# Kernel optimization log

Measured on AMD Instinct MI355X. Metric: run time of the kernel, lower is better.

Reference implementation:

```python
import jax, jax.numpy as jnp
import numpy as np
from jax import lax

B, IN_N, MID_N, OUT_N, K, L, WH = 16, 256, 256, 256, 3, 4096, 1024
EPS = 1e-5


def att_conv(x, W, b=None):
    # x: [B, Cin, L], W: [B, Cout, Cin, K] -> per-sample conv1d, padding='same'
    pl, pr = (K - 1) // 2, K // 2
    xp = jnp.pad(x, ((0, 0), (0, 0), (pl, pr)))
    out = 0.
    for t in range(K):  # small fixed K, unrolled shifted-slice einsum
        out = out + jnp.einsum('bcl,boc->bol', lax.dynamic_slice_in_dim(xp, t, L, 2), W[..., t])
    if b is not None:
        out = out + b[:, :, None]
    return out


def batch_norm(x, w, b):
    # training-mode BN over (N, L) per channel, biased variance
    mean = x.mean((0, 2), keepdims=True)
    var = ((x - mean) ** 2).mean((0, 2), keepdims=True)
    return (x - mean) * (w[None, :, None] / jnp.sqrt(var + EPS)) + b[None, :, None]


def se_module(x, w1, b1, w2, b2):
    s = x.mean(2, keepdims=True)  # [B, C, 1]
    s = jax.nn.relu(jnp.einsum('bcl,oc->bol', s, w1) + b1[None, :, None])
    s = jax.nn.sigmoid(jnp.einsum('bcl,oc->bol', s, w2) + b2[None, :, None])
    return x * s


def setup_inputs() -> dict:
    key = jax.random.key(0)
    ks = jax.random.split(key, 16)
    f = lambda k, sh, sc=0.02: jax.random.normal(k, sh, jnp.float32) * sc
    return {
        'x': f(ks[0], (B, IN_N, L), 1.0),
        'att1': f(ks[1], (B, MID_N, WH), 1.0),
        'att2': f(ks[2], (B, MID_N, WH), 1.0),
        'att3': f(ks[3], (B, OUT_N, WH), 1.0),
        'w1_w': f(ks[4], (IN_N * K, WH)), 'w1_b': jnp.zeros((IN_N * K,), jnp.float32),
        'w2_w': f(ks[5], (MID_N * K, WH)), 'w2_b': jnp.zeros((MID_N * K,), jnp.float32),
        'w3_w': f(ks[6], (MID_N * K, WH)), 'w3_b': jnp.zeros((MID_N * K,), jnp.float32),
        'b1_w': f(ks[7], (1, WH)), 'b1_b': jnp.zeros((1,), jnp.float32),
        'bn2_w': jnp.full((MID_N,), 0.1, jnp.float32), 'bn2_b': jnp.zeros((MID_N,), jnp.float32),
        'bn3_w': jnp.full((OUT_N,), 0.1, jnp.float32), 'bn3_b': jnp.zeros((OUT_N,), jnp.float32),
        'se1_w': f(ks[8], (OUT_N, OUT_N)), 'se1_b': jnp.zeros((OUT_N,), jnp.float32),
        'se2_w': f(ks[9], (OUT_N, OUT_N)), 'se2_b': jnp.zeros((OUT_N,), jnp.float32),
    }


def reference(x, att1, att2, att3, w1_w, w1_b, w2_w, w2_b, w3_w, w3_b,
              b1_w, b1_b, bn2_w, bn2_b, bn3_w, bn3_b, se1_w, se1_b, se2_w, se2_b):
    shortcut = x  # in_n == out_n, no downsample -> Identity
    # hypernetwork weight generation (Linear on last dim)
    W1 = (att1 @ w1_w.T + w1_b).reshape(B, MID_N, IN_N, K)
    W2 = (att2 @ w2_w.T + w2_b).reshape(B, MID_N, MID_N, K)
    W3 = (att3 @ w3_w.T + w3_b).reshape(B, OUT_N, MID_N, K)
    b1 = (att1 @ b1_w.T + b1_b)[..., 0]  # [B, mid_n]
    h = jax.nn.relu(att_conv(x, W1, b1))
    h = jax.nn.relu(batch_norm(att_conv(h, W2), bn2_w, bn2_b))
    h = jax.nn.relu(batch_norm(att_conv(h, W3), bn3_w, bn3_b))
    out = jax.nn.relu(se_module(h, se1_w, se1_b, se2_w, se2_b) + shortcut)
    return out
```

## Files before the change

### kernel.cpp

```cpp
#include <hip/hip_runtime.h>
#include <hip/hip_bf16.h>

using bf16 = __hip_bfloat16;
typedef __attribute__((ext_vector_type(4))) float f32x4;
typedef __attribute__((ext_vector_type(8))) short short8;
typedef __attribute__((ext_vector_type(2))) unsigned int uint2v;
typedef __attribute__((ext_vector_type(4))) unsigned int uint4v;

#define DEVI static __device__ __forceinline__

DEVI unsigned short f2b(float f){
  unsigned int u = __float_as_uint(f);
  unsigned int r = (u + 0x7fffu + ((u >> 16) & 1u)) >> 16;
  return (unsigned short)r;
}
DEVI float b2f(unsigned short u){
  return __uint_as_float(((unsigned int)u) << 16);
}

DEVI void gload16(const void* g, void* l){
  __builtin_amdgcn_global_load_lds(
      (const __attribute__((address_space(1))) unsigned int*)g,
      (__attribute__((address_space(3))) unsigned int*)l, 16, 0, 0);
}

__global__ __launch_bounds__(256) void k_transpose_x(const float* __restrict__ x,
                                                     bf16* __restrict__ xt)
{
  __shared__ float tile[64][65];
  const int b = blockIdx.z, l0 = blockIdx.x*64, c0 = blockIdx.y*64;
  const int tid = threadIdx.x;
  {
    const int r = tid >> 2, q = tid & 3;
    const float* src = x + ((size_t)(b*256 + c0 + r))*4096 + l0 + q*16;
    #pragma unroll
    for (int j = 0; j < 4; ++j){
      const f32x4 v = *reinterpret_cast<const f32x4*>(src + j*4);
      #pragma unroll
      for (int e = 0; e < 4; ++e) tile[r][q*16 + j*4 + e] = v[e];
    }
  }
  __syncthreads();
  {
    const int jr = tid >> 2, cq = tid & 3;
    unsigned int w[8];
    #pragma unroll
    for (int e = 0; e < 8; ++e){
      const float lo = tile[cq*16 + 2*e][jr];
      const float hi = tile[cq*16 + 2*e + 1][jr];
      w[e] = (unsigned int)f2b(lo) | ((unsigned int)f2b(hi) << 16);
    }
    unsigned short* dst = (unsigned short*)xt + ((size_t)b*4098 + l0 + jr + 1)*256 + c0 + cq*16;
    uint4v a0 = {w[0],w[1],w[2],w[3]}, a1 = {w[4],w[5],w[6],w[7]};
    *reinterpret_cast<uint4v*>(dst)     = a0;
    *reinterpret_cast<uint4v*>(dst + 8) = a1;
  }
}

__global__ void k_zero_pads(bf16* __restrict__ xt, bf16* __restrict__ h1t)
{
  const int b = blockIdx.x, tid = threadIdx.x;
  const size_t top = (size_t)b*4098*256 + tid;
  const size_t bot = (size_t)b*4098*256 + (size_t)4097*256 + tid;
  unsigned short* px = (unsigned short*)xt;
  unsigned short* ph = (unsigned short*)h1t;
  px[top] = 0; px[bot] = 0; ph[top] = 0; ph[bot] = 0;
}

__global__ __launch_bounds__(256) void k_cvt3(const float* __restrict__ s0, const float* __restrict__ s1,
                                              const float* __restrict__ s2, bf16* __restrict__ dst, int n1)
{
  const size_t total = (size_t)3 * (size_t)n1 / 4;
  for (size_t i = (size_t)blockIdx.x*256 + threadIdx.x; i < total; i += (size_t)gridDim.x*256){
    const size_t e = i*4;
    const int which = (int)(e / (size_t)n1);
    const size_t off = e - (size_t)which*(size_t)n1;
    const float* s = which==0 ? s0 : which==1 ? s1 : s2;
    const f32x4 v = *reinterpret_cast<const f32x4*>(s + off);
    uint2v p;
    p[0] = (unsigned)f2b(v[0]) | ((unsigned)f2b(v[1])<<16);
    p[1] = (unsigned)f2b(v[2]) | ((unsigned)f2b(v[3])<<16);
    *reinterpret_cast<uint2v*>((unsigned short*)dst + e) = p;
  }
}

__global__ __launch_bounds__(256, 3) void k_gen(const float* __restrict__ att1f, const float* __restrict__ att2f,
                                                const float* __restrict__ att3f, const bf16* __restrict__ wbp,
                                                const float* __restrict__ bias0, const float* __restrict__ bias1,
                                                const float* __restrict__ bias2, bf16* __restrict__ Wt)
{
  __shared__ bf16 sAll[24576];
  const int flat = blockIdx.x + blockIdx.z*64;
  const int xcd = flat & 7, s = flat >> 3;
  const int t = s % 3, u = s / 3;
  const int ch = u & 1;
  const int tau = (u >> 1)*8 + xcd;
  const int i = tau >> 5, boc = tau & 31;
  const int bo0 = boc*128, c0 = ch*128;
  const bf16*  __restrict__ A  = wbp + (size_t)i*768*1024 + (size_t)(c0*3 + t)*1024;
  const float* __restrict__ Bf = ((i==0) ? att1f : (i==1) ? att2f : att3f) + (size_t)bo0*1024;
  const float* __restrict__ bias = (i==0) ? bias0 : (i==1) ? bias1 : bias2;
  const int tid = threadIdx.x, lane = tid & 63, wid = tid >> 6;
  const int wr = wid >> 1, wc = wid & 1;
  const int frow = lane & 15, g = lane >> 4;
  f32x4 acc[4][4] = {};

#define GEN_STAGE(kt, bufi) { \
    _Pragma("unroll") \
    for (int j = 0; j < 2; ++j){ \
      const int q = tid + j*256, r = q >> 2, s3 = q & 3; \
      const int cc = (s3 ^ ((r >> 1) & 3)) * 8; \
      gload16(A + (size_t)r*3072 + (kt)*32 + cc, (char*)sAll + (bufi)*8192 + q*16); \
    } \
    _Pragma("unroll") \
    for (int j = 0; j < 4; ++j){ \
      const int q = tid + j*256, r = q >> 3, s7 = q & 7; \
      const int ss = s7 ^ (r & 7); \
      gload16(Bf + (size_t)r*1024 + (kt)*32 + ss*4, (char*)sAll + 16384 + (bufi)*16384 + q*16); \
    } \
  }

  GEN_STAGE(0, 0);
  #pragma unroll 1
  for (int kt = 0; kt < 32; ++kt){
    const int p = kt & 1;
    if (kt + 1 < 32){
      GEN_STAGE(kt+1, p^1);
      asm volatile("s_waitcnt vmcnt(6)" ::: "memory");
    } else {
      asm volatile("s_waitcnt vmcnt(0)" ::: "memory");
    }
    __builtin_amdgcn_s_barrier();
    const char* pA = (const char*)sAll + p*8192;
    const char* pB = (const char*)sAll + 16384 + p*16384;
    short8 bfr[4];
    #pragma unroll
    for (int n = 0; n < 4; ++n){
      const int row = wc*64 + n*16 + frow;
      const f32x4 f0 = *reinterpret_cast<const f32x4*>(pB + row*128 + (((2*g)  ^ (row & 7))*16));
      const f32x4 f1 = *reinterpret_cast<const f32x4*>(pB + row*128 + (((2*g+1)^ (row & 7))*16));
      unsigned int w0, w1, w2, w3;
      asm("v_cvt_pk_bf16_f32 %0, %1, %2" : "=v"(w0) : "v"(f0[0]), "v"(f0[1]));
      asm("v_cvt_pk_bf16_f32 %0, %1, %2" : "=v"(w1) : "v"(f0[2]), "v"(f0[3]));
      asm("v_cvt_pk_bf16_f32 %0, %1, %2" : "=v"(w2) : "v"(f1[0]), "v"(f1[1]));
      asm("v_cvt_pk_bf16_f32 %0, %1, %2" : "=v"(w3) : "v"(f1[2]), "v"(f1[3]));
      union { uint4v u; short8 sv; } cvtu;
      cvtu.u[0] = w0; cvtu.u[1] = w1; cvtu.u[2] = w2; cvtu.u[3] = w3;
      bfr[n] = cvtu.sv;
    }
    __builtin_amdgcn_s_setprio(1);
    #pragma unroll
    for (int m = 0; m < 4; ++m){
      const int row = wr*64 + m*16 + frow;
      const int sl = g ^ ((row >> 1) & 3);
      const short8 af = *reinterpret_cast<const short8*>(pA + row*64 + sl*16);
      #pragma unroll
      for (int n = 0; n < 4; ++n)
        acc[m][n] = __builtin_amdgcn_mfma_f32_16x16x32_bf16(af, bfr[n], acc[m][n], 0, 0, 0);
    }
    __builtin_amdgcn_s_setprio(0);
    __builtin_amdgcn_s_barrier();
  }
#undef GEN_STAGE

  #pragma unroll
  for (int m = 0; m < 4; ++m){
    const int lcol = wr*64 + m*16 + g*4;
    float bi[4];
    #pragma unroll
    for (int j = 0; j < 4; ++j) bi[j] = bias[(c0 + lcol + j)*3 + t];
    #pragma unroll
    for (int n = 0; n < 4; ++n){
      const int row = wc*64 + n*16 + frow;
      uint2v pk;
      pk[0] = (unsigned)f2b(acc[m][n][0] + bi[0]) | ((unsigned)f2b(acc[m][n][1] + bi[1]) << 16);
      pk[1] = (unsigned)f2b(acc[m][n][2] + bi[2]) | ((unsigned)f2b(acc[m][n][3] + bi[3]) << 16);
      const int chunk = (lcol >> 3) ^ (row & 15);
      *reinterpret_cast<uint2v*>((char*)sAll + row*256 + chunk*16 + (g&1)*8) = pk;
    }
  }
  __syncthreads();
  {
    const int bb = boc >> 1, o0 = (boc & 1)*128;
    char* gp = (char*)Wt + 2*(((((size_t)(i*16 + bb)*3 + t)*256 + o0)*256) + c0);
    #pragma unroll
    for (int it = 0; it < 8; ++it){
      const int row = it*16 + (tid >> 4);
      const int c = tid & 15;
      const int cs2 = c ^ (row & 15);
      const uint4v v = *reinterpret_cast<const uint4v*>((const char*)sAll + row*256 + cs2*16);
      *reinterpret_cast<uint4v*>(gp + (size_t)row*512 + c*16) = v;
    }
  }
}

__global__ __launch_bounds__(256) void k_b1(const float* __restrict__ att1, const float* __restrict__ b1w,
                                            const float* __restrict__ b1b, float* __restrict__ out)
{
  const int m = blockIdx.x*4 + (threadIdx.x >> 6);
  const int lane = threadIdx.x & 63;
  const float* a = att1 + (size_t)m*1024;
  float s = 0.f;
  for (int k = lane*4; k < 1024; k += 256){
    const f32x4 v = *reinterpret_cast<const f32x4*>(a + k);
    const f32x4 w = *reinterpret_cast<const f32x4*>(b1w + k);
    s += v[0]*w[0] + v[1]*w[1] + v[2]*w[2] + v[3]*w[3];
  }
  #pragma unroll
  for (int d = 32; d > 0; d >>= 1) s += __shfl_down(s, d);
  if (lane == 0) out[m] = s + b1b[0];
}

__global__ __launch_bounds__(512, 4) void k_conv(const bf16* __restrict__ Xt, const bf16* __restrict__ W,
                                                 const float* __restrict__ bias, bf16* __restrict__ out,
                                                 int outBatchStride, int outRowOff, int applyRelu,
                                                 float* __restrict__ statSum, float* __restrict__ statSq)
{
  __shared__ bf16 sAll[32768];
  const int flat = blockIdx.x + (blockIdx.z << 5);
  const int xcd = flat & 7, slot = flat >> 3;
  const int b = 2*xcd + (slot >> 5);
  const int l0 = (slot & 31) * 128;
  const int tid = threadIdx.x, lane = tid & 63, wid = tid >> 6;
  const int wr = wid >> 1, wc = wid & 1;
  const int frow = lane & 15, g = lane >> 4;
  f32x4 acc[4][4] = {};

#define CONV_STAGE(kt, bufi) { \
    const int ct3 = (kt)/3, tt = (kt) - ct3*3, c0 = ct3*32; \
    const bf16* Ab = W  + (((size_t)b*3 + tt)*256)*256 + c0; \
    const bf16* Bb = Xt + ((size_t)b*4098 + l0 + tt)*256 + c0; \
    _Pragma("unroll") \
    for (int j = 0; j < 2; ++j){ \
      const int q = tid + j*512, r = q >> 2, s3 = q & 3; \
      const int cc = (s3 ^ ((r >> 1) & 3)) * 8; \
      gload16(Ab + (size_t)r*256 + cc, &sAll[(bufi)*8192 + q*8]); \
    } \
    { const int q = tid, r = q >> 2, s3 = q & 3; \
      const int cc = (s3 ^ ((r >> 1) & 3)) * 8; \
      gload16(Bb + (size_t)r*256 + cc, &sAll[16384 + (bufi)*4096 + q*8]); } \
  }

  CONV_STAGE(0, 0);
  #pragma unroll 1
  for (int kt = 0; kt < 24; ++kt){
    const int buf = kt & 1;
    if (kt + 1 < 24){
      CONV_STAGE(kt+1, buf^1);
      asm volatile("s_waitcnt vmcnt(3)" ::: "memory");
    } else {
      asm volatile("s_waitcnt vmcnt(0)" ::: "memory");
    }
    __builtin_amdgcn_s_barrier();
    const bf16* pA = sAll + buf*8192;
    const bf16* pB = sAll + 16384 + buf*4096;
    short8 bfr[4], afr[4];
    #pragma unroll
    for (int n = 0; n < 4; ++n){
      const int row = wc*64 + n*16 + frow;
      const int sl = g ^ ((row >> 1) & 3);
      bfr[n] = *reinterpret_cast<const short8*>(pB + row*32 + sl*8);
    }
    #pragma unroll
    for (int m = 0; m < 4; ++m){
      const int row = wr*64 + m*16 + frow;
      const int sl = g ^ ((row >> 1) & 3);
      afr[m] = *reinterpret_cast<const short8*>(pA + row*32 + sl*8);
    }
    __builtin_amdgcn_s_setprio(1);
    #pragma unroll
    for (int m = 0; m < 4; ++m)
      #pragma unroll
      for (int n = 0; n < 4; ++n)
        acc[m][n] = __builtin_amdgcn_mfma_f32_16x16x32_bf16(afr[m], bfr[n], acc[m][n], 0, 0, 0);
    __builtin_amdgcn_s_setprio(0);
    __builtin_amdgcn_s_barrier();
  }
#undef CONV_STAGE

  float cs[4][4] = {{0.f}}, cq[4][4] = {{0.f}};
  #pragma unroll
  for (int m = 0; m < 4; ++m){
    const int col = wr*64 + m*16 + g*4;
    float bi[4] = {0.f, 0.f, 0.f, 0.f};
    if (bias){
      const f32x4 bv = *reinterpret_cast<const f32x4*>(bias + b*256 + col);
      bi[0]=bv[0]; bi[1]=bv[1]; bi[2]=bv[2]; bi[3]=bv[3];
    }
    #pragma unroll
    for (int n = 0; n < 4; ++n){
      const int row = wc*64 + n*16 + frow;
      float v[4];
      #pragma unroll
      for (int j = 0; j < 4; ++j){
        v[j] = acc[m][n][j] + bi[j];
        if (applyRelu) v[j] = fmaxf(v[j], 0.f);
        cs[m][j] += v[j];
        cq[m][j] += v[j]*v[j];
      }
      uint2v pk;
      pk[0] = (unsigned)f2b(v[0]) | ((unsigned)f2b(v[1]) << 16);
      pk[1] = (unsigned)f2b(v[2]) | ((unsigned)f2b(v[3]) << 16);
      const int chunk = (col >> 3) ^ (row & 31);
      *reinterpret_cast<uint2v*>((char*)sAll + row*512 + chunk*16 + (g&1)*8) = pk;
    }
  }
  __syncthreads();
  {
    char* gp = (char*)out + 2*((size_t)b*outBatchStride + (size_t)(l0 + outRowOff)*256);
    #pragma unroll
    for (int it = 0; it < 8; ++it){
      const int row = it*16 + (tid >> 5);
      const int c = tid & 31;
      const int cs2 = c ^ (row & 31);
      const uint4v v = *reinterpret_cast<const uint4v*>((const char*)sAll + row*512 + cs2*16);
      *reinterpret_cast<uint4v*>(gp + (size_t)row*512 + c*16) = v;
    }
  }
  if (statSum){
    #pragma unroll
    for (int m = 0; m < 4; ++m)
      #pragma unroll
      for (int j = 0; j < 4; ++j){
        #pragma unroll
        for (int d = 1; d < 16; d <<= 1){
          cs[m][j] += __shfl_xor(cs[m][j], d);
          cq[m][j] += __shfl_xor(cq[m][j], d);
        }
      }
    __syncthreads();
    float* ls = (float*)sAll;
    float* lq = ls + 512;
    if (frow == 0){
      #pragma unroll
      for (int m = 0; m < 4; ++m)
        #pragma unroll
        for (int j = 0; j < 4; ++j){
          ls[wid*64 + m*16 + g*4 + j] = cs[m][j];
          lq[wid*64 + m*16 + g*4 + j] = cq[m][j];
        }
    }
    __syncthreads();
    if (tid < 256){
      const int o = tid, wrI = o >> 6, idx = o & 63;
      const float s  = ls[(wrI*2 + 0)*64 + idx] + ls[(wrI*2 + 1)*64 + idx];
      const float qq = lq[(wrI*2 + 0)*64 + idx] + lq[(wrI*2 + 1)*64 + idx];
      atomicAdd(statSum + o, s);
      atomicAdd(statSq  + o, qq);
    }
  }
}

__global__ void k_bnfin(const float* __restrict__ sum, const float* __restrict__ sq,
                        const float* __restrict__ g, const float* __restrict__ bb,
                        float* __restrict__ scale, float* __restrict__ shift)
{
  const int o = threadIdx.x;
  const float inv = 1.f/65536.f;
  const float m = sum[o]*inv;
  const float v = fmaxf(sq[o]*inv - m*m, 0.f);
  const float sc = g[o] / sqrtf(v + 1e-5f);
  scale[o] = sc;
  shift[o] = bb[o] - m*sc;
}

__global__ __launch_bounds__(256) void k_norm2(const bf16* __restrict__ y, const float* __restrict__ scale,
                                               const float* __restrict__ shift, bf16* __restrict__ h)
{
  const int gr = blockIdx.x*8 + (threadIdx.x >> 5);
  const int oc = threadIdx.x & 31;
  const int b = gr / 4098, lp = gr - b*4098;
  unsigned short* dst = (unsigned short*)h + (size_t)gr*256 + oc*8;
  if (lp == 0 || lp == 4097){
    uint4v z = {0u,0u,0u,0u};
    *reinterpret_cast<uint4v*>(dst) = z;
    return;
  }
  const unsigned short* src = (const unsigned short*)y + ((size_t)b*4096 + (lp-1))*256 + oc*8;
  const uint4v in = *reinterpret_cast<const uint4v*>(src);
  const f32x4 sA0 = *reinterpret_cast<const f32x4*>(scale + oc*8);
  const f32x4 sA1 = *reinterpret_cast<const f32x4*>(scale + oc*8 + 4);
  const f32x4 hA0 = *reinterpret_cast<const f32x4*>(shift + oc*8);
  const f32x4 hA1 = *reinterpret_cast<const f32x4*>(shift + oc*8 + 4);
  uint4v ov;
  #pragma unroll
  for (int e = 0; e < 4; ++e){
    const unsigned int w = in[e];
    const float sc0 = (e<2) ? sA0[2*e] : sA1[2*e-4];
    const float sc1 = (e<2) ? sA0[2*e+1] : sA1[2*e-3];
    const float sh0 = (e<2) ? hA0[2*e] : hA1[2*e-4];
    const float sh1 = (e<2) ? hA0[2*e+1] : hA1[2*e-3];
    const float v0 = fmaxf(b2f((unsigned short)(w & 0xffffu))*sc0 + sh0, 0.f);
    const float v1 = fmaxf(b2f((unsigned short)(w >> 16))*sc1 + sh1, 0.f);
    ov[e] = (unsigned)f2b(v0) | ((unsigned)f2b(v1) << 16);
  }
  *reinterpret_cast<uint4v*>(dst) = ov;
}

__global__ __launch_bounds__(256) void k_norm3(bf16* __restrict__ y, const float* __restrict__ scale,
                                               const float* __restrict__ shift, float* __restrict__ s_sum)
{
  __shared__ float red[8][256];
  const int tid = threadIdx.x;
  const int rr = tid >> 5, oc = tid & 31;
  const size_t row = (size_t)blockIdx.x*8 + rr;
  const int b = (int)(row >> 12);
  unsigned short* p = (unsigned short*)y + row*256 + oc*8;
  const uint4v in = *reinterpret_cast<const uint4v*>(p);
  const f32x4 sA0 = *reinterpret_cast<const f32x4*>(scale + oc*8);
  const f32x4 sA1 = *reinterpret_cast<const f32x4*>(scale + oc*8 + 4);
  const f32x4 hA0 = *reinterpret_cast<const f32x4*>(shift + oc*8);
  const f32x4 hA1 = *reinterpret_cast<const f32x4*>(shift + oc*8 + 4);
  uint4v ov;
  float loc[8];
  #pragma unroll
  for (int e = 0; e < 4; ++e){
    const unsigned int w = in[e];
    const float sc0 = (e<2) ? sA0[2*e] : sA1[2*e-4];
    const float sc1 = (e<2) ? sA0[2*e+1] : sA1[2*e-3];
    const float sh0 = (e<2) ? hA0[2*e] : hA1[2*e-4];
    const float sh1 = (e<2) ? hA0[2*e+1] : hA1[2*e-3];
    const float v0 = fmaxf(b2f((unsigned short)(w & 0xffffu))*sc0 + sh0, 0.f);
    const float v1 = fmaxf(b2f((unsigned short)(w >> 16))*sc1 + sh1, 0.f);
    loc[2*e] = v0; loc[2*e+1] = v1;
    ov[e] = (unsigned)f2b(v0) | ((unsigned)f2b(v1) << 16);
  }
  *reinterpret_cast<uint4v*>(p) = ov;
  #pragma unroll
  for (int j = 0; j < 8; ++j) red[rr][oc*8 + j] = loc[j];
  __syncthreads();
  const int o = tid;
  float tot = 0.f;
  #pragma unroll
  for (int r2 = 0; r2 < 8; ++r2) tot += red[r2][o];
  atomicAdd(&s_sum[(size_t)b*256 + o], tot);
}

__global__ __launch_bounds__(256) void k_se(const float* __restrict__ s_sum, const float* __restrict__ w1,
                                            const float* __restrict__ b1, const float* __restrict__ w2,
                                            const float* __restrict__ b2, float* __restrict__ s2)
{
  __shared__ float sv[256];
  __shared__ float t1[256];
  const int b = blockIdx.x, o = threadIdx.x;
  sv[o] = s_sum[(size_t)b*256 + o] * (1.f/4096.f);
  __syncthreads();
  float a = b1[o];
  for (int c = 0; c < 256; ++c) a += w1[(size_t)o*256 + c] * sv[c];
  t1[o] = fmaxf(a, 0.f);
  __syncthreads();
  float a2 = b2[o];
  for (int c = 0; c < 256; ++c) a2 += w2[(size_t)o*256 + c] * t1[c];
  s2[(size_t)b*256 + o] = 1.f / (1.f + expf(-a2));
}

__global__ __launch_bounds__(256) void k_final(const bf16* __restrict__ h3, const float* __restrict__ s2,
                                               const float* __restrict__ x, float* __restrict__ out)
{
  __shared__ float tile[64][65];
  const int b = blockIdx.z, o0 = blockIdx.y*64, l0 = blockIdx.x*64;
  const int tid = threadIdx.x;
  {
    const int r = tid >> 2, q = tid & 3;
    const unsigned short* src = (const unsigned short*)h3 + ((size_t)b*4096 + l0 + r)*256 + o0 + q*16;
    const uint4v a0 = *reinterpret_cast<const uint4v*>(src);
    const uint4v a1 = *reinterpret_cast<const uint4v*>(src + 8);
    #pragma unroll
    for (int e = 0; e < 4; ++e){
      tile[r][q*16 + 2*e]         = b2f((unsigned short)(a0[e] & 0xffffu));
      tile[r][q*16 + 2*e + 1]     = b2f((unsigned short)(a0[e] >> 16));
      tile[r][q*16 + 8 + 2*e]     = b2f((unsigned short)(a1[e] & 0xffffu));
      tile[r][q*16 + 8 + 2*e + 1] = b2f((unsigned short)(a1[e] >> 16));
    }
  }
  __syncthreads();
  {
    const int orow = tid >> 2, q = tid & 3;
    const int o = o0 + orow;
    const float sc = s2[(size_t)b*256 + o];
    const float* xs = x + ((size_t)b*256 + o)*4096 + l0 + q*16;
    float* dst = out + ((size_t)b*256 + o)*4096 + l0 + q*16;
    #pragma unroll
    for (int k = 0; k < 16; k += 4){
      const f32x4 xv = *reinterpret_cast<const f32x4*>(xs + k);
      f32x4 r;
      #pragma unroll
      for (int e = 0; e < 4; ++e)
        r[e] = fmaxf(tile[q*16 + k + e][orow]*sc + xv[e], 0.f);
      *reinterpret_cast<f32x4*>(dst + k) = r;
    }
  }
}

extern "C" void kernel_launch(void* const* d_in, const int* in_sizes, int n_in,
                              void* d_out, int out_size, void* d_ws, size_t ws_size,
                              hipStream_t stream)
{
  const float* x     = (const float*)d_in[0];
  const float* att1  = (const float*)d_in[1];
  const float* att2  = (const float*)d_in[2];
  const float* att3  = (const float*)d_in[3];
  const float* w1_w  = (const float*)d_in[4];
  const float* w1_b  = (const float*)d_in[5];
  const float* w2_w  = (const float*)d_in[6];
  const float* w2_b  = (const float*)d_in[7];
  const float* w3_w  = (const float*)d_in[8];
  const float* w3_b  = (const float*)d_in[9];
  const float* b1_w  = (const float*)d_in[10];
  const float* b1_b  = (const float*)d_in[11];
  const float* bn2_w = (const float*)d_in[12];
  const float* bn2_b = (const float*)d_in[13];
  const float* bn3_w = (const float*)d_in[14];
  const float* bn3_b = (const float*)d_in[15];
  const float* se1_w = (const float*)d_in[16];
  const float* se1_b = (const float*)d_in[17];
  const float* se2_w = (const float*)d_in[18];
  const float* se2_b = (const float*)d_in[19];

  char* ws = (char*)d_ws;
  bf16*  xT   = (bf16*)(ws + 0);
  bf16*  h1T  = (bf16*)(ws + 33570816);
  bf16*  y2T  = (bf16*)(ws + 67141632);
  bf16*  h2T  = (bf16*)(ws + 100696064);
  bf16*  Wt   = (bf16*)(ws + 134266880);
  bf16*  wb   = (bf16*)(ws + 178307072);
  float* b1v  = (float*)(ws + 183025664);
  float* st   = (float*)(ws + 183042048);
  float* bn2sum = st;
  float* bn2sq  = st + 256;
  float* bn3sum = st + 512;
  float* bn3sq  = st + 768;
  float* s_sum  = st + 1024;
  float* scale2 = st + 5120;
  float* shift2 = st + 5376;
  float* scale3 = st + 5632;
  float* shift3 = st + 5888;
  float* s2v    = st + 6144;
  bf16*  y3T  = (bf16*)(ws + 0);

  hipMemsetAsync(st, 0, 5120*sizeof(float), stream);

  k_transpose_x<<<dim3(64,4,16),256,0,stream>>>(x, xT);
  k_zero_pads<<<16,256,0,stream>>>(xT, h1T);
  k_cvt3<<<512,256,0,stream>>>(w1_w, w2_w, w3_w, wb, 768*1024);
  k_gen<<<dim3(64,1,9),256,0,stream>>>(att1, att2, att3, wb, w1_b, w2_b, w3_b, Wt);
  k_b1<<<1024,256,0,stream>>>(att1, b1_w, b1_b, b1v);

  k_conv<<<dim3(32,1,16),512,0,stream>>>(xT,  Wt,                           b1v,     h1T, 4098*256, 1, 1, nullptr, nullptr);
  k_conv<<<dim3(32,1,16),512,0,stream>>>(h1T, Wt + (size_t)1*16*3*256*256,  nullptr, y2T, 4096*256, 0, 0, bn2sum, bn2sq);
  k_bnfin<<<1,256,0,stream>>>(bn2sum, bn2sq, bn2_w, bn2_b, scale2, shift2);
  k_norm2<<<8196,256,0,stream>>>(y2T, scale2, shift2, h2T);
  k_conv<<<dim3(32,1,16),512,0,stream>>>(h2T, Wt + (size_t)2*16*3*256*256,  nullptr, y3T, 4096*256, 0, 0, bn3sum, bn3sq);
  k_bnfin<<<1,256,0,stream>>>(bn3sum, bn3sq, bn3_w, bn3_b, scale3, shift3);
  k_norm3<<<8192,256,0,stream>>>(y3T, scale3, shift3, s_sum);
  k_se<<<16,256,0,stream>>>(s_sum, se1_w, se1_b, se2_w, se2_b, s2v);
  k_final<<<dim3(64,4,16),256,0,stream>>>((const bf16*)y3T, s2v, x, (float*)d_out);
}
```

Measured before the change: 309.2 us.

## Retile conv to 128x128 output halves with 3-tap shared X tile, fuse BN3 into final

The conv kernel now uses 256-thread blocks, each computing a 128-channel half of the output. It loads all three tap weight slices plus one X tile with a two-row halo per channel chunk, so the three taps reuse the same shifted X data instead of staging it separately per tap. That means 8 outer iterations with 48 MFMAs each instead of 24 with 16, at the cost of larger LDS use (about 66KB) and more registers. Separately, k_norm3 no longer writes normalized values back; BN3 scale/shift is applied inside k_final, and the residual is read from the bf16 transposed x (xT) instead of the fp32 x. This removes one write pass but reads the shortcut at reduced precision.

```diff
diff --git a/kernel.cpp b/kernel.cpp
--- a/kernel.cpp
+++ b/kernel.cpp
@@ -211,68 +211,86 @@
   if (lane == 0) out[m] = s + b1b[0];
 }
 
-__global__ __launch_bounds__(512, 4) void k_conv(const bf16* __restrict__ Xt, const bf16* __restrict__ W,
+__global__ __launch_bounds__(256, 2) void k_conv(const bf16* __restrict__ Xt, const bf16* __restrict__ W,
                                                  const float* __restrict__ bias, bf16* __restrict__ out,
                                                  int outBatchStride, int outRowOff, int applyRelu,
                                                  float* __restrict__ statSum, float* __restrict__ statSq)
 {
-  __shared__ bf16 sAll[32768];
-  const int flat = blockIdx.x + (blockIdx.z << 5);
-  const int xcd = flat & 7, slot = flat >> 3;
-  const int b = 2*xcd + (slot >> 5);
-  const int l0 = (slot & 31) * 128;
+  __shared__ char sAll[67584];
+  const int flat = blockIdx.x + (blockIdx.z << 6);
+  const int xcd = flat & 7, s = flat >> 3;
+  const int b = 2*xcd + (s >> 6);
+  const int rem = s & 63;
+  const int oh = rem >> 5;
+  const int l0 = (rem & 31) * 128;
   const int tid = threadIdx.x, lane = tid & 63, wid = tid >> 6;
   const int wr = wid >> 1, wc = wid & 1;
   const int frow = lane & 15, g = lane >> 4;
   f32x4 acc[4][4] = {};
 
-#define CONV_STAGE(kt, bufi) { \
-    const int ct3 = (kt)/3, tt = (kt) - ct3*3, c0 = ct3*32; \
-    const bf16* Ab = W  + (((size_t)b*3 + tt)*256)*256 + c0; \
-    const bf16* Bb = Xt + ((size_t)b*4098 + l0 + tt)*256 + c0; \
+#define CONV_STAGE(ct, bufi) { \
+    const bf16* Ab = W + (((size_t)b*3)*256 + oh*128)*256 + (ct)*32; \
+    _Pragma("unroll") \
+    for (int t = 0; t < 3; ++t){ \
+      _Pragma("unroll") \
+      for (int j = 0; j < 2; ++j){ \
+        const int q = tid + j*256, r = q >> 2; \
+        const int cc = ((q & 3) ^ ((r >> 1) & 3)) * 8; \
+        gload16(Ab + (size_t)t*65536 + (size_t)r*256 + cc, \
+                sAll + (bufi)*24576 + t*8192 + q*16); \
+      } \
+    } \
+    const bf16* Bb = Xt + ((size_t)b*4098 + l0)*256 + (ct)*32; \
     _Pragma("unroll") \
     for (int j = 0; j < 2; ++j){ \
-      const int q = tid + j*512, r = q >> 2, s3 = q & 3; \
-      const int cc = (s3 ^ ((r >> 1) & 3)) * 8; \
-      gload16(Ab + (size_t)r*256 + cc, &sAll[(bufi)*8192 + q*8]); \
+      const int q = tid + j*256, r = q >> 2; \
+      const int cc = ((q & 3) ^ ((r >> 1) & 3)) * 8; \
+      gload16(Bb + (size_t)r*256 + cc, sAll + 49152 + (bufi)*9216 + q*16); \
     } \
-    { const int q = tid, r = q >> 2, s3 = q & 3; \
-      const int cc = (s3 ^ ((r >> 1) & 3)) * 8; \
-      gload16(Bb + (size_t)r*256 + cc, &sAll[16384 + (bufi)*4096 + q*8]); } \
+    {  \
+      const int q = 512 + (tid & 63), r = q >> 2; \
+      const int cc = ((q & 3) ^ ((r >> 1) & 3)) * 8; \
+      gload16(Bb + (size_t)r*256 + cc, sAll + 49152 + (bufi)*9216 + q*16); \
+    } \
   }
 
   CONV_STAGE(0, 0);
   #pragma unroll 1
-  for (int kt = 0; kt < 24; ++kt){
-    const int buf = kt & 1;
-    if (kt + 1 < 24){
-      CONV_STAGE(kt+1, buf^1);
-      asm volatile("s_waitcnt vmcnt(3)" ::: "memory");
+  for (int ct = 0; ct < 8; ++ct){
+    const int buf = ct & 1;
+    if (ct + 1 < 8){
+      CONV_STAGE(ct+1, buf^1);
+      asm volatile("s_waitcnt vmcnt(9)" ::: "memory");
     } else {
       asm volatile("s_waitcnt vmcnt(0)" ::: "memory");
     }
     __builtin_amdgcn_s_barrier();
-    const bf16* pA = sAll + buf*8192;
-    const bf16* pB = sAll + 16384 + buf*4096;
-    short8 bfr[4], afr[4];
-    #pragma unroll
-    for (int n = 0; n < 4; ++n){
-      const int row = wc*64 + n*16 + frow;
-      const int sl = g ^ ((row >> 1) & 3);
-      bfr[n] = *reinterpret_cast<const short8*>(pB + row*32 + sl*8);
-    }
-    #pragma unroll
-    for (int m = 0; m < 4; ++m){
-      const int row = wr*64 + m*16 + frow;
-      const int sl = g ^ ((row >> 1) & 3);
-      afr[m] = *reinterpret_cast<const short8*>(pA + row*32 + sl*8);
+    const char* pA = sAll + buf*24576;
+    const char* pB = sAll + 49152 + buf*9216;
+    short8 afr[3][4], bfr[3][4];
+    #pragma unroll
+    for (int t = 0; t < 3; ++t){
+      #pragma unroll
+      for (int m = 0; m < 4; ++m){
+        const int row = wr*64 + m*16 + frow;
+        const int sl = g ^ ((row >> 1) & 3);
+        afr[t][m] = *reinterpret_cast<const short8*>(pA + t*8192 + row*64 + sl*16);
+      }
+      #pragma unroll
+      for (int n = 0; n < 4; ++n){
+        const int rl = wc*64 + n*16 + frow + t;
+        const int sl = g ^ ((rl >> 1) & 3);
+        bfr[t][n] = *reinterpret_cast<const short8*>(pB + rl*64 + sl*16);
+      }
     }
     __builtin_amdgcn_s_setprio(1);
     #pragma unroll
-    for (int m = 0; m < 4; ++m)
-      #pragma unroll
-      for (int n = 0; n < 4; ++n)
-        acc[m][n] = __builtin_amdgcn_mfma_f32_16x16x32_bf16(afr[m], bfr[n], acc[m][n], 0, 0, 0);
+    for (int t = 0; t < 3; ++t)
+      #pragma unroll
+      for (int m = 0; m < 4; ++m)
+        #pragma unroll
+        for (int n = 0; n < 4; ++n)
+          acc[m][n] = __builtin_amdgcn_mfma_f32_16x16x32_bf16(afr[t][m], bfr[t][n], acc[m][n], 0, 0, 0);
     __builtin_amdgcn_s_setprio(0);
     __builtin_amdgcn_s_barrier();
   }
@@ -281,10 +299,10 @@
   float cs[4][4] = {{0.f}}, cq[4][4] = {{0.f}};
   #pragma unroll
   for (int m = 0; m < 4; ++m){
-    const int col = wr*64 + m*16 + g*4;
+    const int ol = wr*64 + m*16 + g*4;
     float bi[4] = {0.f, 0.f, 0.f, 0.f};
     if (bias){
-      const f32x4 bv = *reinterpret_cast<const f32x4*>(bias + b*256 + col);
+      const f32x4 bv = *reinterpret_cast<const f32x4*>(bias + b*256 + oh*128 + ol);
       bi[0]=bv[0]; bi[1]=bv[1]; bi[2]=bv[2]; bi[3]=bv[3];
     }
     #pragma unroll
@@ -301,19 +319,19 @@
       uint2v pk;
       pk[0] = (unsigned)f2b(v[0]) | ((unsigned)f2b(v[1]) << 16);
       pk[1] = (unsigned)f2b(v[2]) | ((unsigned)f2b(v[3]) << 16);
-      const int chunk = (col >> 3) ^ (row & 31);
-      *reinterpret_cast<uint2v*>((char*)sAll + row*512 + chunk*16 + (g&1)*8) = pk;
+      const int chunk = (ol >> 3) ^ (row & 15);
+      *reinterpret_cast<uint2v*>(sAll + row*256 + chunk*16 + (g&1)*8) = pk;
     }
   }
   __syncthreads();
   {
-    char* gp = (char*)out + 2*((size_t)b*outBatchStride + (size_t)(l0 + outRowOff)*256);
+    char* gp = (char*)out + 2*((size_t)b*outBatchStride + (size_t)(l0 + outRowOff)*256 + oh*128);
     #pragma unroll
     for (int it = 0; it < 8; ++it){
-      const int row = it*16 + (tid >> 5);
-      const int c = tid & 31;
-      const int cs2 = c ^ (row & 31);
-      const uint4v v = *reinterpret_cast<const uint4v*>((const char*)sAll + row*512 + cs2*16);
+      const int row = it*16 + (tid >> 4);
+      const int c = tid & 15;
+      const int cs2 = c ^ (row & 15);
+      const uint4v v = *reinterpret_cast<const uint4v*>((const char*)sAll + row*256 + cs2*16);
       *reinterpret_cast<uint4v*>(gp + (size_t)row*512 + c*16) = v;
     }
   }
@@ -330,7 +348,7 @@
       }
     __syncthreads();
     float* ls = (float*)sAll;
-    float* lq = ls + 512;
+    float* lq = ls + 256;
     if (frow == 0){
       #pragma unroll
       for (int m = 0; m < 4; ++m)
@@ -341,12 +359,12 @@
         }
     }
     __syncthreads();
-    if (tid < 256){
-      const int o = tid, wrI = o >> 6, idx = o & 63;
-      const float s  = ls[(wrI*2 + 0)*64 + idx] + ls[(wrI*2 + 1)*64 + idx];
-      const float qq = lq[(wrI*2 + 0)*64 + idx] + lq[(wrI*2 + 1)*64 + idx];
-      atomicAdd(statSum + o, s);
-      atomicAdd(statSq  + o, qq);
+    if (tid < 128){
+      const int ol = tid, wrI = ol >> 6, idx = ol & 63;
+      const float sv = ls[(wrI*2 + 0)*64 + idx] + ls[(wrI*2 + 1)*64 + idx];
+      const float qv = lq[(wrI*2 + 0)*64 + idx] + lq[(wrI*2 + 1)*64 + idx];
+      atomicAdd(statSum + oh*128 + ol, sv);
+      atomicAdd(statSq  + oh*128 + ol, qv);
     }
   }
 }
@@ -397,21 +415,20 @@
   *reinterpret_cast<uint4v*>(dst) = ov;
 }
 
-__global__ __launch_bounds__(256) void k_norm3(bf16* __restrict__ y, const float* __restrict__ scale,
-                                               const float* __restrict__ shift, float* __restrict__ s_sum)
+__global__ __launch_bounds__(256) void k_sum3(const bf16* __restrict__ y, const float* __restrict__ scale,
+                                              const float* __restrict__ shift, float* __restrict__ s_sum)
 {
   __shared__ float red[8][256];
   const int tid = threadIdx.x;
   const int rr = tid >> 5, oc = tid & 31;
   const size_t row = (size_t)blockIdx.x*8 + rr;
   const int b = (int)(row >> 12);
-  unsigned short* p = (unsigned short*)y + row*256 + oc*8;
+  const unsigned short* p = (const unsigned short*)y + row*256 + oc*8;
   const uint4v in = *reinterpret_cast<const uint4v*>(p);
   const f32x4 sA0 = *reinterpret_cast<const f32x4*>(scale + oc*8);
   const f32x4 sA1 = *reinterpret_cast<const f32x4*>(scale + oc*8 + 4);
   const f32x4 hA0 = *reinterpret_cast<const f32x4*>(shift + oc*8);
   const f32x4 hA1 = *reinterpret_cast<const f32x4*>(shift + oc*8 + 4);
-  uint4v ov;
   float loc[8];
   #pragma unroll
   for (int e = 0; e < 4; ++e){
@@ -420,12 +437,9 @@
     const float sc1 = (e<2) ? sA0[2*e+1] : sA1[2*e-3];
     const float sh0 = (e<2) ? hA0[2*e] : hA1[2*e-4];
     const float sh1 = (e<2) ? hA0[2*e+1] : hA1[2*e-3];
-    const float v0 = fmaxf(b2f((unsigned short)(w & 0xffffu))*sc0 + sh0, 0.f);
-    const float v1 = fmaxf(b2f((unsigned short)(w >> 16))*sc1 + sh1, 0.f);
-    loc[2*e] = v0; loc[2*e+1] = v1;
-    ov[e] = (unsigned)f2b(v0) | ((unsigned)f2b(v1) << 16);
-  }
-  *reinterpret_cast<uint4v*>(p) = ov;
+    loc[2*e]   = fmaxf(b2f((unsigned short)(w & 0xffffu))*sc0 + sh0, 0.f);
+    loc[2*e+1] = fmaxf(b2f((unsigned short)(w >> 16))*sc1 + sh1, 0.f);
+  }
   #pragma unroll
   for (int j = 0; j < 8; ++j) red[rr][oc*8 + j] = loc[j];
   __syncthreads();
@@ -454,39 +468,63 @@
   s2[(size_t)b*256 + o] = 1.f / (1.f + expf(-a2));
 }
 
-__global__ __launch_bounds__(256) void k_final(const bf16* __restrict__ h3, const float* __restrict__ s2,
-                                               const float* __restrict__ x, float* __restrict__ out)
-{
-  __shared__ float tile[64][65];
+__global__ __launch_bounds__(256) void k_final(const bf16* __restrict__ y3, const bf16* __restrict__ xt,
+                                               const float* __restrict__ scale, const float* __restrict__ shift,
+                                               const float* __restrict__ s2, float* __restrict__ out)
+{
+  __shared__ float tH[64][65];
+  __shared__ float tX[64][65];
   const int b = blockIdx.z, o0 = blockIdx.y*64, l0 = blockIdx.x*64;
   const int tid = threadIdx.x;
   {
     const int r = tid >> 2, q = tid & 3;
-    const unsigned short* src = (const unsigned short*)h3 + ((size_t)b*4096 + l0 + r)*256 + o0 + q*16;
-    const uint4v a0 = *reinterpret_cast<const uint4v*>(src);
-    const uint4v a1 = *reinterpret_cast<const uint4v*>(src + 8);
+    const int cb = o0 + q*16;
+    const unsigned short* sy = (const unsigned short*)y3 + ((size_t)b*4096 + l0 + r)*256 + cb;
+    const unsigned short* sx = (const unsigned short*)xt + ((size_t)b*4098 + l0 + r + 1)*256 + cb;
+    const uint4v y0 = *reinterpret_cast<const uint4v*>(sy);
+    const uint4v y1 = *reinterpret_cast<const uint4v*>(sy + 8);
+    const uint4v x0 = *reinterpret_cast<const uint4v*>(sx);
+    const uint4v x1 = *reinterpret_cast<const uint4v*>(sx + 8);
+    const f32x4 sc0 = *reinterpret_cast<const f32x4*>(scale + cb);
+    const f32x4 sc1 = *reinterpret_cast<const f32x4*>(scale + cb + 4);
+    const f32x4 sc2 = *reinterpret_cast<const f32x4*>(scale + cb + 8);
+    const f32x4 sc3 = *reinterpret_cast<const f32x4*>(scale + cb + 12);
+    const f32x4 sh0 = *reinterpret_cast<const f32x4*>(shift + cb);
+    const f32x4 sh1 = *reinterpret_cast<const f32x4*>(shift + cb + 4);
+    const f32x4 sh2 = *reinterpret_cast<const f32x4*>(shift + cb + 8);
+    const f32x4 sh3 = *reinterpret_cast<const f32x4*>(shift + cb + 12);
     #pragma unroll
     for (int e = 0; e < 4; ++e){
-      tile[r][q*16 + 2*e]         = b2f((unsigned short)(a0[e] & 0xffffu));
-      tile[r][q*16 + 2*e + 1]     = b2f((unsigned short)(a0[e] >> 16));
-      tile[r][q*16 + 8 + 2*e]     = b2f((unsigned short)(a1[e] & 0xffffu));
-      tile[r][q*16 + 8 + 2*e + 1] = b2f((unsigned short)(a1[e] >> 16));
+      const float a0 = (e<2) ? sc0[2*e] : sc1[2*e-4];
+      const float a1 = (e<2) ? sc0[2*e+1] : sc1[2*e-3];
+      const float b0 = (e<2) ? sh0[2*e] : sh1[2*e-4];
+      const float b1v = (e<2) ? sh0[2*e+1] : sh1[2*e-3];
+      tH[r][q*16 + 2*e]     = fmaxf(b2f((unsigned short)(y0[e] & 0xffffu))*a0 + b0, 0.f);
+      tH[r][q*16 + 2*e + 1] = fmaxf(b2f((unsigned short)(y0[e] >> 16))*a1 + b1v, 0.f);
+      tX[r][q*16 + 2*e]     = b2f((unsigned short)(x0[e] & 0xffffu));
+      tX[r][q*16 + 2*e + 1] = b2f((unsigned short)(x0[e] >> 16));
+      const float c0v = (e<2) ? sc2[2*e] : sc3[2*e-4];
+      const float c1v = (e<2) ? sc2[2*e+1] : sc3[2*e-3];
+      const float d0 = (e<2) ? sh2[2*e] : sh3[2*e-4];
+      const float d1 = (e<2) ? sh2[2*e+1] : sh3[2*e-3];
+      tH[r][q*16 + 8 + 2*e]     = fmaxf(b2f((unsigned short)(y1[e] & 0xffffu))*c0v + d0, 0.f);
+      tH[r][q*16 + 8 + 2*e + 1] = fmaxf(b2f((unsigned short)(y1[e] >> 16))*c1v + d1, 0.f);
+      tX[r][q*16 + 8 + 2*e]     = b2f((unsigned short)(x1[e] & 0xffffu));
+      tX[r][q*16 + 8 + 2*e + 1] = b2f((unsigned short)(x1[e] >> 16));
     }
   }
   __syncthreads();
   {
     const int orow = tid >> 2, q = tid & 3;
     const int o = o0 + orow;
-    const float sc = s2[(size_t)b*256 + o];
-    const float* xs = x + ((size_t)b*256 + o)*4096 + l0 + q*16;
+    const float sfac = s2[(size_t)b*256 + o];
     float* dst = out + ((size_t)b*256 + o)*4096 + l0 + q*16;
     #pragma unroll
     for (int k = 0; k < 16; k += 4){
-      const f32x4 xv = *reinterpret_cast<const f32x4*>(xs + k);
       f32x4 r;
       #pragma unroll
       for (int e = 0; e < 4; ++e)
-        r[e] = fmaxf(tile[q*16 + k + e][orow]*sc + xv[e], 0.f);
+        r[e] = fmaxf(tH[q*16 + k + e][orow]*sfac + tX[q*16 + k + e][orow], 0.f);
       *reinterpret_cast<f32x4*>(dst + k) = r;
     }
   }
@@ -536,7 +574,7 @@
   float* scale3 = st + 5632;
   float* shift3 = st + 5888;
   float* s2v    = st + 6144;
-  bf16*  y3T  = (bf16*)(ws + 0);
+  bf16*  y3T  = (bf16*)(ws + 33570816);
 
   hipMemsetAsync(st, 0, 5120*sizeof(float), stream);
 
@@ -546,13 +584,13 @@
   k_gen<<<dim3(64,1,9),256,0,stream>>>(att1, att2, att3, wb, w1_b, w2_b, w3_b, Wt);
   k_b1<<<1024,256,0,stream>>>(att1, b1_w, b1_b, b1v);
 
-  k_conv<<<dim3(32,1,16),512,0,stream>>>(xT,  Wt,                           b1v,     h1T, 4098*256, 1, 1, nullptr, nullptr);
-  k_conv<<<dim3(32,1,16),512,0,stream>>>(h1T, Wt + (size_t)1*16*3*256*256,  nullptr, y2T, 4096*256, 0, 0, bn2sum, bn2sq);
+  k_conv<<<dim3(64,1,16),256,0,stream>>>(xT,  Wt,                           b1v,     h1T, 4098*256, 1, 1, nullptr, nullptr);
+  k_conv<<<dim3(64,1,16),256,0,stream>>>(h1T, Wt + (size_t)1*16*3*256*256,  nullptr, y2T, 4096*256, 0, 0, bn2sum, bn2sq);
   k_bnfin<<<1,256,0,stream>>>(bn2sum, bn2sq, bn2_w, bn2_b, scale2, shift2);
   k_norm2<<<8196,256,0,stream>>>(y2T, scale2, shift2, h2T);
-  k_conv<<<dim3(32,1,16),512,0,stream>>>(h2T, Wt + (size_t)2*16*3*256*256,  nullptr, y3T, 4096*256, 0, 0, bn3sum, bn3sq);
+  k_conv<<<dim3(64,1,16),256,0,stream>>>(h2T, Wt + (size_t)2*16*3*256*256,  nullptr, y3T, 4096*256, 0, 0, bn3sum, bn3sq);
   k_bnfin<<<1,256,0,stream>>>(bn3sum, bn3sq, bn3_w, bn3_b, scale3, shift3);
-  k_norm3<<<8192,256,0,stream>>>(y3T, scale3, shift3, s_sum);
+  k_sum3<<<8192,256,0,stream>>>(y3T, scale3, shift3, s_sum);
   k_se<<<16,256,0,stream>>>(s_sum, se1_w, se1_b, se2_w, se2_b, s2v);
-  k_final<<<dim3(64,4,16),256,0,stream>>>((const bf16*)y3T, s2v, x, (float*)d_out);
-}
+  k_final<<<dim3(64,4,16),256,0,stream>>>(y3T, xT, scale3, shift3, s2v, (float*)d_out);
+}
```

Measured after the change: 297.6 us (median of 3 runs). 3.8% less time.
